# Kernel tuning notes

Hardware: AMD Instinct MI355X
Metric: run time of the kernel (lower is better)

The kernel has to match this reference:

```python
import jax, jax.numpy as jnp
import numpy as np

N_STATIONS = 35
N_PER_ST = 12
N_NODES = N_STATIONS * N_PER_ST   # 420
MAX_EDGES = 5120                  # true edge count = 34 * 12^2 = 4896
MAX_SUPER = 65536                 # true superedge candidates = 33*12*144 = 57024
PI = float(np.pi)

# constraint rows (r, phi, z) from the torch module
C_LO = jnp.array([269.0, -3.15, -2386.0], dtype=jnp.float32)
C_HI = jnp.array([581.0, 3.15, 2386.0], dtype=jnp.float32)


def _calc_dphi(p1, p2):
    d = p2 - p1
    d = jnp.where(d > PI, d - 2.0 * PI, d)
    return jnp.where(d < -PI, d + 2.0 * PI, d)


def _norm_node(v, k):
    return 2.0 * (v - C_LO[k]) / (C_HI[k] - C_LO[k]) - 1.0


def _norm_edge(v, k):
    return 2.0 * v / (C_HI[k] - C_LO[k])


def setup_inputs() -> dict:
    rng = np.random.default_rng(0)
    r = rng.uniform(270.0, 580.0, N_NODES)
    phi = rng.uniform(-3.1, 3.1, N_NODES)
    z = rng.uniform(-2000.0, 2000.0, N_NODES)
    station = np.arange(N_NODES) // N_PER_ST
    track = np.arange(N_NODES) % N_PER_ST  # one hit per track per station
    data = np.stack([
        np.zeros(N_NODES),          # event
        r * np.sin(phi),            # x (so atan2(x, y) = phi)
        r * np.cos(phi),            # y
        z,                          # z
        station.astype(np.float64),
        track.astype(np.float64),
        np.arange(N_NODES, dtype=np.float64),  # index_old
    ], axis=1).astype(np.float32)
    return {"event_data": jnp.asarray(data)}


def reference(event_data):
    x, y, z = event_data[:, 1], event_data[:, 2], event_data[:, 3]
    station, track, index_old = event_data[:, 4], event_data[:, 5], event_data[:, 6]
    # convert() : cartesian -> cylindrical (x<-r, y<-phi)
    r = jnp.sqrt(x * x + y * y)
    phi = jnp.arctan2(x, y)
    # get_graph(): adjacency of consecutive stations, row-major nonzero like torch
    adj = station[:, None] == (station[None, :] - 1.0)
    i_idx, j_idx = jnp.nonzero(adj, size=MAX_EDGES, fill_value=0)
    e_valid = jnp.arange(MAX_EDGES) < jnp.sum(adj)
    phi_p, phi_c = phi[i_idx], phi[j_idx]
    z_p, z_c = z[i_idx], z[j_idx]
    r_p, r_c = r[i_idx], r[j_idx]
    io_p, io_c = index_old[i_idx], index_old[j_idx]
    is_true = track[i_idx] == track[j_idx]  # torch leaves is_true uninitialized; defined as same-track
    dphi = _calc_dphi(phi_p, phi_c)
    dz, dx = z_c - z_p, r_c - r_p
    ez = (station[i_idx] + 1.0) / N_STATIONS
    e_index = jnp.arange(MAX_EDGES, dtype=event_data.dtype)
    # normalize() node-mode on endpoint phi/z (the only normalized cols used later) and edge-mode on dx,dy,dz
    yp_n, yc_n = _norm_node(phi_p, 1), _norm_node(phi_c, 1)
    zp_n, zc_n = _norm_node(z_p, 2), _norm_node(z_c, 2)
    dx_n, dy_n, dz_n = _norm_edge(dx, 0), _norm_edge(dphi, 1), _norm_edge(dz, 2)
    # apply_edge_restriction (masking instead of compaction)
    e_keep = e_valid & (dy_n > -10.0) & (dy_n < 10.0) & (dz_n > -10.0) & (dz_n < 10.0)
    # get_edges_from_supernodes: join first.index_old_c == second.index_old_p
    eq = (io_c[:, None] == io_p[None, :]) & e_keep[:, None] & e_keep[None, :]
    si, sj = jnp.nonzero(eq, size=MAX_SUPER, fill_value=0)
    s_valid = jnp.arange(MAX_SUPER) < jnp.sum(eq)
    d_first = jnp.stack([dx_n[si], dy_n[si], dz_n[si]], -1)
    d_second = jnp.stack([dx_n[sj], dy_n[sj], dz_n[sj]], -1)
    weight = jnp.linalg.norm(d_first - d_second, axis=1)
    # apply_weight_restriction: compact, order-preserving
    s_keep = s_valid & (weight < 0.1)
    (k_idx,) = jnp.nonzero(s_keep, size=MAX_SUPER, fill_value=0)
    k_valid = jnp.arange(MAX_SUPER) < jnp.sum(s_keep)
    fi, se = si[k_idx], sj[k_idx]
    su_is_true = is_true[fi] & is_true[se]
    su_ioc = jnp.where(k_valid, e_index[fi], -2.0)  # superedge index_old_c = first edge's index
    su_iop = jnp.where(k_valid, e_index[se], -2.0)  # superedge index_old_p = second edge's index
    su_y = jnp.where(k_valid, su_is_true.astype(event_data.dtype), 0.0)
    # construct_output_graph: nodes = (filtered) edges, edges = superedges
    node_idx = jnp.where(e_keep, e_index, -1.0)
    X = jnp.where(e_keep[:, None], jnp.stack([yp_n, yc_n, zp_n, zc_n, ez], -1), 0.0)
    Ri = node_idx[:, None] == su_ioc[None, :]   # [MAX_EDGES, MAX_SUPER] bool
    Ro = node_idx[:, None] == su_iop[None, :]
    super_ids = jnp.stack([su_iop, su_ioc], -1)
    edge_ids = jnp.where(e_keep[:, None], jnp.stack([io_p, io_c, e_index], -1), -1.0)
    return X, Ri, Ro, su_y, super_ids, node_idx, edge_ids
```

## Files before the change

kernel.cpp:

```cpp
#include <hip/hip_runtime.h>
#include <math.h>

#define NND 420
#define MAXE 5120
#define MAXS 65536

#define OFF_X    ((size_t)0)
#define OFF_RI   ((size_t)25600)
#define OFF_RO   ((size_t)25600 + 335544320)
#define OFF_SUY  ((size_t)671114240)
#define OFF_SIDS ((size_t)671179776)
#define OFF_NIDX ((size_t)671310848)
#define OFF_EIDS ((size_t)671315968)
#define OUT_TOTAL ((size_t)671331328)

static __device__ __forceinline__ float f32(double d) { return (float)d; }

__device__ float g_dxn[MAXE], g_dyn[MAXE], g_dzn[MAXE];
__device__ float g_iop[MAXE], g_ioc[MAXE];
__device__ int   g_keep[MAXE], g_istrue[MAXE], g_jn[MAXE];
__device__ int   g_estart[NND + 1];
__device__ int   g_cnt2[MAXE], g_off2[MAXE];
__device__ int   g_nedges, g_nkeep;

__global__ __launch_bounds__(512) void kA(const float* __restrict__ ev,
                                          float* __restrict__ out) {
    __shared__ float s_r[NND], s_phi[NND], s_z[NND], s_st[NND], s_trk[NND], s_io[NND];
    __shared__ int   s_cnt[NND];
    __shared__ int   s_off[NND + 1];
    __shared__ short s_ei[MAXE], s_ej[MAXE];

    const float PI_F  = f32(3.141592653589793);
    const float TPI_F = f32(6.283185307179586);
    const float LO1 = -3.15f, SPAN1 = 3.15f + 3.15f;
    const float LO2 = -2386.0f, SPAN2 = 4772.0f;
    const float SPAN0 = 312.0f;

    int t = threadIdx.x;
    for (int n = t; n < NND; n += 512) {
        float x = ev[n * 7 + 1], y = ev[n * 7 + 2];
        s_z[n]   = ev[n * 7 + 3];
        s_st[n]  = ev[n * 7 + 4];
        s_trk[n] = ev[n * 7 + 5];
        s_io[n]  = ev[n * 7 + 6];
        s_r[n]   = sqrtf(__fadd_rn(__fmul_rn(x, x), __fmul_rn(y, y)));
        s_phi[n] = atan2f(x, y);
    }
    __syncthreads();

    for (int i = t; i < NND; i += 512) {
        float target = s_st[i] + 1.0f;
        int c = 0;
        for (int j = 0; j < NND; ++j) c += (s_st[j] == target) ? 1 : 0;
        s_cnt[i] = c;
    }
    __syncthreads();
    if (t == 0) {
        int acc = 0;
        for (int i = 0; i < NND; ++i) { s_off[i] = acc; acc += s_cnt[i]; }
        s_off[NND] = acc;
        g_nedges = acc;
        for (int n = 0; n <= NND; ++n)
            g_estart[n] = (s_off[n] > MAXE) ? MAXE : s_off[n];
    }
    __syncthreads();

    for (int i = t; i < NND; i += 512) {
        float target = s_st[i] + 1.0f;
        int k = s_off[i];
        for (int j = 0; j < NND; ++j) {
            if (s_st[j] == target) {
                if (k < MAXE) { s_ei[k] = (short)i; s_ej[k] = (short)j; }
                ++k;
            }
        }
    }
    __syncthreads();

    int nedges = s_off[NND]; if (nedges > MAXE) nedges = MAXE;

    for (int k = t; k < MAXE; k += 512) {
        bool valid = (k < nedges);
        int i = valid ? (int)s_ei[k] : 0;
        int j = valid ? (int)s_ej[k] : 0;
        float phip = s_phi[i], phic = s_phi[j];
        float zp = s_z[i], zc = s_z[j];
        float rp = s_r[i], rc = s_r[j];
        float iop = s_io[i], ioc = s_io[j];
        int istrue = (s_trk[i] == s_trk[j]) ? 1 : 0;

        float d = __fsub_rn(phic, phip);
        if (d >  PI_F) d = __fsub_rn(d, TPI_F);
        if (d < -PI_F) d = __fadd_rn(d, TPI_F);

        float dzv = __fsub_rn(zc, zp);
        float dxv = __fsub_rn(rc, rp);
        float dxn = __fdiv_rn(__fmul_rn(2.0f, dxv), SPAN0);
        float dyn = __fdiv_rn(__fmul_rn(2.0f, d),   SPAN1);
        float dzn = __fdiv_rn(__fmul_rn(2.0f, dzv), SPAN2);

        bool keep = valid && (dyn > -10.0f) && (dyn < 10.0f)
                          && (dzn > -10.0f) && (dzn < 10.0f);

        float ypn = __fsub_rn(__fdiv_rn(__fmul_rn(2.0f, __fsub_rn(phip, LO1)), SPAN1), 1.0f);
        float ycn = __fsub_rn(__fdiv_rn(__fmul_rn(2.0f, __fsub_rn(phic, LO1)), SPAN1), 1.0f);
        float zpn = __fsub_rn(__fdiv_rn(__fmul_rn(2.0f, __fsub_rn(zp, LO2)), SPAN2), 1.0f);
        float zcn = __fsub_rn(__fdiv_rn(__fmul_rn(2.0f, __fsub_rn(zc, LO2)), SPAN2), 1.0f);
        float ez  = __fdiv_rn(__fadd_rn(s_st[i], 1.0f), 35.0f);

        if (keep) {
            size_t oX = OFF_X + (size_t)k * 5;
            out[oX + 0] = ypn; out[oX + 1] = ycn; out[oX + 2] = zpn;
            out[oX + 3] = zcn; out[oX + 4] = ez;
        }
        out[OFF_NIDX + (size_t)k] = keep ? (float)k : -1.0f;
        size_t oE = OFF_EIDS + (size_t)k * 3;
        out[oE + 0] = keep ? iop : -1.0f;
        out[oE + 1] = keep ? ioc : -1.0f;
        out[oE + 2] = keep ? (float)k : -1.0f;

        g_dxn[k] = dxn; g_dyn[k] = dyn; g_dzn[k] = dzn;
        g_iop[k] = iop; g_ioc[k] = ioc;
        g_keep[k] = keep ? 1 : 0; g_istrue[k] = istrue; g_jn[k] = j;
    }
}

__global__ __launch_bounds__(256) void kB() {
    int a = blockIdx.x * 256 + threadIdx.x;
    if (a >= MAXE) return;
    int c = 0;
    if (g_keep[a]) {
        int jn = g_jn[a];
        float ioca = g_ioc[a];
        float a0 = g_dxn[a], a1 = g_dyn[a], a2 = g_dzn[a];
        int b0 = g_estart[jn], b1 = g_estart[jn + 1];
        for (int b = b0; b < b1; ++b) {
            if (g_keep[b] && (g_iop[b] == ioca)) {
                float d0 = __fsub_rn(a0, g_dxn[b]);
                float d1 = __fsub_rn(a1, g_dyn[b]);
                float d2 = __fsub_rn(a2, g_dzn[b]);
                float w = sqrtf(__fadd_rn(__fadd_rn(__fmul_rn(d0, d0),
                                                    __fmul_rn(d1, d1)),
                                          __fmul_rn(d2, d2)));
                if (w < 0.1f) ++c;
            }
        }
    }
    g_cnt2[a] = c;
}

__global__ __launch_bounds__(1024) void kC() {
    __shared__ int part[1024];
    int t = threadIdx.x;
    int v[5]; int s = 0;
#pragma unroll
    for (int q = 0; q < 5; ++q) { v[q] = g_cnt2[t * 5 + q]; s += v[q]; }
    part[t] = s;
    __syncthreads();
    for (int off = 1; off < 1024; off <<= 1) {
        int x = (t >= off) ? part[t - off] : 0;
        __syncthreads();
        part[t] += x;
        __syncthreads();
    }
    int run = part[t] - s;
#pragma unroll
    for (int q = 0; q < 5; ++q) { g_off2[t * 5 + q] = run; run += v[q]; }
    if (t == 1023) g_nkeep = part[1023];
}

__global__ __launch_bounds__(256) void kD(float* __restrict__ out) {
    int a = blockIdx.x * 256 + threadIdx.x;
    if (a >= MAXE) return;
    if (!g_keep[a]) return;
    int pos = g_off2[a];
    int jn = g_jn[a];
    float ioca = g_ioc[a];
    float a0 = g_dxn[a], a1 = g_dyn[a], a2 = g_dzn[a];
    int b0 = g_estart[jn], b1 = g_estart[jn + 1];
    for (int b = b0; b < b1; ++b) {
        if (g_keep[b] && (g_iop[b] == ioca)) {
            float d0 = __fsub_rn(a0, g_dxn[b]);
            float d1 = __fsub_rn(a1, g_dyn[b]);
            float d2 = __fsub_rn(a2, g_dzn[b]);
            float w = sqrtf(__fadd_rn(__fadd_rn(__fmul_rn(d0, d0),
                                                __fmul_rn(d1, d1)),
                                      __fmul_rn(d2, d2)));
            if (w < 0.1f) {
                if (pos < MAXS) {
                    out[OFF_SUY + (size_t)pos] =
                        (g_istrue[a] && g_istrue[b]) ? 1.0f : 0.0f;
                    size_t os = OFF_SIDS + (size_t)pos * 2;
                    out[os + 0] = (float)b;
                    out[os + 1] = (float)a;
                    out[OFF_RI + (size_t)a * MAXS + (size_t)pos] = 1.0f;
                    out[OFF_RO + (size_t)b * MAXS + (size_t)pos] = 1.0f;
                }
                ++pos;
            }
        }
    }
}

__global__ __launch_bounds__(256) void kE(float* __restrict__ out) {
    int p = blockIdx.x * 256 + threadIdx.x;
    if (p >= MAXS) return;
    if (p >= g_nkeep) {
        size_t os = OFF_SIDS + (size_t)p * 2;
        out[os + 0] = -2.0f;
        out[os + 1] = -2.0f;
    }
}

extern "C" void kernel_launch(void* const* d_in, const int* in_sizes, int n_in,
                              void* d_out, int out_size, void* d_ws, size_t ws_size,
                              hipStream_t stream) {
    const float* ev = (const float*)d_in[0];
    float* out = (float*)d_out;

    hipMemsetAsync(d_out, 0, (size_t)out_size * sizeof(float), stream);

    hipLaunchKernelGGL(kA, dim3(1), dim3(512), 0, stream, ev, out);
    hipLaunchKernelGGL(kB, dim3((MAXE + 255) / 256), dim3(256), 0, stream);
    hipLaunchKernelGGL(kC, dim3(1), dim3(1024), 0, stream);
    hipLaunchKernelGGL(kD, dim3((MAXE + 255) / 256), dim3(256), 0, stream, out);
    hipLaunchKernelGGL(kE, dim3((MAXS + 255) / 256), dim3(256), 0, stream, out);
}
```

Baseline: 2.618 ms.

## Fuse pipeline into one cooperative kernel with in-kernel zero-fill and wave-parallel superedges

Replaces the memset and five kernels with a single cooperative kernel separated by grid syncs. Block 0 builds the edges while the other blocks zero the ~2.7GB output with float4 stores, writing -2 directly into the super_ids region so the separate fill kernel is no longer needed. Superedge counting and emission move from one thread per edge to one wave per edge, using ballot and popcount to compact positions. The output writes are still dominated by the memset-sized store volume, and grid.sync plus using 1023 blocks for the fill may or may not match hipMemset bandwidth.

```diff
diff --git a/kernel.cpp b/kernel.cpp
--- a/kernel.cpp
+++ b/kernel.cpp
@@ -1,5 +1,8 @@
 #include <hip/hip_runtime.h>
+#include <hip/hip_cooperative_groups.h>
 #include <math.h>
+
+namespace cg = cooperative_groups;
 
 #define NND 420
 #define MAXE 5120
@@ -7,28 +10,35 @@
 
 #define OFF_X    ((size_t)0)
 #define OFF_RI   ((size_t)25600)
-#define OFF_RO   ((size_t)25600 + 335544320)
+#define OFF_RO   ((size_t)(25600 + 335544320))
 #define OFF_SUY  ((size_t)671114240)
 #define OFF_SIDS ((size_t)671179776)
 #define OFF_NIDX ((size_t)671310848)
 #define OFF_EIDS ((size_t)671315968)
-#define OUT_TOTAL ((size_t)671331328)
+
+typedef float f4 __attribute__((ext_vector_type(4)));
 
 static __device__ __forceinline__ float f32(double d) { return (float)d; }
 
-__device__ float g_dxn[MAXE], g_dyn[MAXE], g_dzn[MAXE];
-__device__ float g_iop[MAXE], g_ioc[MAXE];
-__device__ int   g_keep[MAXE], g_istrue[MAXE], g_jn[MAXE];
+__device__ float g_phi[NND], g_z[NND], g_st[NND];
+__device__ short g_ei[MAXE], g_ej[MAXE];
 __device__ int   g_estart[NND + 1];
+__device__ float g_dxn[MAXE], g_dyn[MAXE], g_dzn[MAXE], g_iop[MAXE], g_ioc[MAXE];
+__device__ int   g_keep[MAXE], g_istrue[MAXE];
 __device__ int   g_cnt2[MAXE], g_off2[MAXE];
-__device__ int   g_nedges, g_nkeep;
-
-__global__ __launch_bounds__(512) void kA(const float* __restrict__ ev,
-                                          float* __restrict__ out) {
+__device__ int   g_ne;
+
+#define GRID_BLOCKS 1024
+#define NWAVES ((GRID_BLOCKS * 256) >> 6)
+
+__global__ __launch_bounds__(256, 4) void kCoop(const float* __restrict__ ev,
+                                                float* __restrict__ out, int n4) {
+    cg::grid_group grid = cg::this_grid();
+
     __shared__ float s_r[NND], s_phi[NND], s_z[NND], s_st[NND], s_trk[NND], s_io[NND];
-    __shared__ int   s_cnt[NND];
-    __shared__ int   s_off[NND + 1];
+    __shared__ int   s_scan[NND];
     __shared__ short s_ei[MAXE], s_ej[MAXE];
+    __shared__ int   s_part[256];
 
     const float PI_F  = f32(3.141592653589793);
     const float TPI_F = f32(6.283185307179586);
@@ -36,179 +46,201 @@
     const float LO2 = -2386.0f, SPAN2 = 4772.0f;
     const float SPAN0 = 312.0f;
 
-    int t = threadIdx.x;
-    for (int n = t; n < NND; n += 512) {
-        float x = ev[n * 7 + 1], y = ev[n * 7 + 2];
-        s_z[n]   = ev[n * 7 + 3];
-        s_st[n]  = ev[n * 7 + 4];
-        s_trk[n] = ev[n * 7 + 5];
-        s_io[n]  = ev[n * 7 + 6];
-        s_r[n]   = sqrtf(__fadd_rn(__fmul_rn(x, x), __fmul_rn(y, y)));
-        s_phi[n] = atan2f(x, y);
-    }
-    __syncthreads();
-
-    for (int i = t; i < NND; i += 512) {
-        float target = s_st[i] + 1.0f;
+    const int t   = threadIdx.x;
+    const int bid = blockIdx.x;
+
+    if (bid == 0) {
+        for (int n = t; n < NND; n += 256) {
+            float x = ev[n * 7 + 1], y = ev[n * 7 + 2];
+            s_r[n]   = sqrtf(__fadd_rn(__fmul_rn(x, x), __fmul_rn(y, y)));
+            s_phi[n] = atan2f(x, y);
+            s_z[n]   = ev[n * 7 + 3];
+            s_st[n]  = ev[n * 7 + 4];
+            s_trk[n] = ev[n * 7 + 5];
+            s_io[n]  = ev[n * 7 + 6];
+        }
+        __syncthreads();
+        for (int i = t; i < NND; i += 256) {
+            float target = s_st[i] + 1.0f;
+            int c = 0;
+            for (int j = 0; j < NND; ++j) c += (s_st[j] == target) ? 1 : 0;
+            s_scan[i] = c;
+        }
+        __syncthreads();
+        if (t == 0) {
+            int acc = 0;
+            for (int i = 0; i < NND; ++i) {
+                int c = s_scan[i];
+                s_scan[i] = acc;
+                g_estart[i] = acc > MAXE ? MAXE : acc;
+                acc += c;
+            }
+            g_estart[NND] = acc > MAXE ? MAXE : acc;
+            g_ne = acc > MAXE ? MAXE : acc;
+        }
+        __syncthreads();
+        for (int i = t; i < NND; i += 256) {
+            float target = s_st[i] + 1.0f;
+            int k = s_scan[i];
+            for (int j = 0; j < NND; ++j) {
+                if (s_st[j] == target) {
+                    if (k < MAXE) { s_ei[k] = (short)i; s_ej[k] = (short)j; }
+                    ++k;
+                }
+            }
+        }
+        __syncthreads();
+        const int ne = g_ne;
+        for (int k = t; k < MAXE; k += 256) {
+            bool valid = (k < ne);
+            int i = valid ? (int)s_ei[k] : 0;
+            int j = valid ? (int)s_ej[k] : 0;
+            float phip = s_phi[i], phic = s_phi[j];
+            float zp = s_z[i], zc = s_z[j];
+            float rp = s_r[i], rc = s_r[j];
+
+            float d = __fsub_rn(phic, phip);
+            if (d >  PI_F) d = __fsub_rn(d, TPI_F);
+            if (d < -PI_F) d = __fadd_rn(d, TPI_F);
+
+            float dzv = __fsub_rn(zc, zp);
+            float dxv = __fsub_rn(rc, rp);
+            float dxn = __fdiv_rn(__fmul_rn(2.0f, dxv), SPAN0);
+            float dyn = __fdiv_rn(__fmul_rn(2.0f, d),   SPAN1);
+            float dzn = __fdiv_rn(__fmul_rn(2.0f, dzv), SPAN2);
+
+            bool keep = valid && (dyn > -10.0f) && (dyn < 10.0f)
+                              && (dzn > -10.0f) && (dzn < 10.0f);
+
+            g_dxn[k] = dxn; g_dyn[k] = dyn; g_dzn[k] = dzn;
+            g_iop[k] = s_io[i]; g_ioc[k] = s_io[j];
+            g_keep[k] = keep ? 1 : 0;
+            g_istrue[k] = (s_trk[i] == s_trk[j]) ? 1 : 0;
+            g_ei[k] = valid ? s_ei[k] : (short)0;
+            g_ej[k] = valid ? s_ej[k] : (short)0;
+        }
+        for (int n = t; n < NND; n += 256) {
+            g_phi[n] = s_phi[n]; g_z[n] = s_z[n]; g_st[n] = s_st[n];
+        }
+    } else {
+        const size_t LOq = OFF_SIDS >> 2;
+        const size_t HIq = (OFF_SIDS + 2 * (size_t)MAXS) >> 2;
+        f4* p = (f4*)out;
+        const f4 z = {0.f, 0.f, 0.f, 0.f};
+        const f4 m = {-2.f, -2.f, -2.f, -2.f};
+        size_t i = (size_t)(bid - 1) * 256 + t;
+        const size_t stride = (size_t)(GRID_BLOCKS - 1) * 256;
+        for (; i < (size_t)n4; i += stride)
+            p[i] = (i >= LOq && i < HIq) ? m : z;
+    }
+    grid.sync();
+
+    const int gtid = bid * 256 + t;
+    const int wid = gtid >> 6, lane = gtid & 63;
+    const int ne = g_ne;
+    for (int a = wid; a < MAXE; a += NWAVES) {
+        bool akeep = (a < ne) && (g_keep[a] != 0);
         int c = 0;
-        for (int j = 0; j < NND; ++j) c += (s_st[j] == target) ? 1 : 0;
-        s_cnt[i] = c;
-    }
-    __syncthreads();
-    if (t == 0) {
-        int acc = 0;
-        for (int i = 0; i < NND; ++i) { s_off[i] = acc; acc += s_cnt[i]; }
-        s_off[NND] = acc;
-        g_nedges = acc;
-        for (int n = 0; n <= NND; ++n)
-            g_estart[n] = (s_off[n] > MAXE) ? MAXE : s_off[n];
-    }
-    __syncthreads();
-
-    for (int i = t; i < NND; i += 512) {
-        float target = s_st[i] + 1.0f;
-        int k = s_off[i];
-        for (int j = 0; j < NND; ++j) {
-            if (s_st[j] == target) {
-                if (k < MAXE) { s_ei[k] = (short)i; s_ej[k] = (short)j; }
-                ++k;
-            }
-        }
-    }
-    __syncthreads();
-
-    int nedges = s_off[NND]; if (nedges > MAXE) nedges = MAXE;
-
-    for (int k = t; k < MAXE; k += 512) {
-        bool valid = (k < nedges);
-        int i = valid ? (int)s_ei[k] : 0;
-        int j = valid ? (int)s_ej[k] : 0;
-        float phip = s_phi[i], phic = s_phi[j];
-        float zp = s_z[i], zc = s_z[j];
-        float rp = s_r[i], rc = s_r[j];
-        float iop = s_io[i], ioc = s_io[j];
-        int istrue = (s_trk[i] == s_trk[j]) ? 1 : 0;
-
-        float d = __fsub_rn(phic, phip);
-        if (d >  PI_F) d = __fsub_rn(d, TPI_F);
-        if (d < -PI_F) d = __fadd_rn(d, TPI_F);
-
-        float dzv = __fsub_rn(zc, zp);
-        float dxv = __fsub_rn(rc, rp);
-        float dxn = __fdiv_rn(__fmul_rn(2.0f, dxv), SPAN0);
-        float dyn = __fdiv_rn(__fmul_rn(2.0f, d),   SPAN1);
-        float dzn = __fdiv_rn(__fmul_rn(2.0f, dzv), SPAN2);
-
-        bool keep = valid && (dyn > -10.0f) && (dyn < 10.0f)
-                          && (dzn > -10.0f) && (dzn < 10.0f);
-
-        float ypn = __fsub_rn(__fdiv_rn(__fmul_rn(2.0f, __fsub_rn(phip, LO1)), SPAN1), 1.0f);
-        float ycn = __fsub_rn(__fdiv_rn(__fmul_rn(2.0f, __fsub_rn(phic, LO1)), SPAN1), 1.0f);
-        float zpn = __fsub_rn(__fdiv_rn(__fmul_rn(2.0f, __fsub_rn(zp, LO2)), SPAN2), 1.0f);
-        float zcn = __fsub_rn(__fdiv_rn(__fmul_rn(2.0f, __fsub_rn(zc, LO2)), SPAN2), 1.0f);
-        float ez  = __fdiv_rn(__fadd_rn(s_st[i], 1.0f), 35.0f);
-
-        if (keep) {
-            size_t oX = OFF_X + (size_t)k * 5;
-            out[oX + 0] = ypn; out[oX + 1] = ycn; out[oX + 2] = zpn;
-            out[oX + 3] = zcn; out[oX + 4] = ez;
-        }
-        out[OFF_NIDX + (size_t)k] = keep ? (float)k : -1.0f;
-        size_t oE = OFF_EIDS + (size_t)k * 3;
-        out[oE + 0] = keep ? iop : -1.0f;
-        out[oE + 1] = keep ? ioc : -1.0f;
-        out[oE + 2] = keep ? (float)k : -1.0f;
-
-        g_dxn[k] = dxn; g_dyn[k] = dyn; g_dzn[k] = dzn;
-        g_iop[k] = iop; g_ioc[k] = ioc;
-        g_keep[k] = keep ? 1 : 0; g_istrue[k] = istrue; g_jn[k] = j;
-    }
-}
-
-__global__ __launch_bounds__(256) void kB() {
-    int a = blockIdx.x * 256 + threadIdx.x;
-    if (a >= MAXE) return;
-    int c = 0;
-    if (g_keep[a]) {
-        int jn = g_jn[a];
+        float ioca = 0.f, a0 = 0.f, a1 = 0.f, a2 = 0.f;
+        if (akeep) {
+            int jn = (int)g_ej[a];
+            int b0 = g_estart[jn], b1 = g_estart[jn + 1];
+            ioca = g_ioc[a]; a0 = g_dxn[a]; a1 = g_dyn[a]; a2 = g_dzn[a];
+            for (int cs = b0; cs < b1; cs += 64) {
+                int b = cs + lane;
+                bool pred = false;
+                if (b < b1 && g_keep[b] && (g_iop[b] == ioca)) {
+                    float d0 = __fsub_rn(a0, g_dxn[b]);
+                    float d1 = __fsub_rn(a1, g_dyn[b]);
+                    float d2 = __fsub_rn(a2, g_dzn[b]);
+                    float w = sqrtf(__fadd_rn(__fadd_rn(__fmul_rn(d0, d0),
+                                                        __fmul_rn(d1, d1)),
+                                              __fmul_rn(d2, d2)));
+                    pred = (w < 0.1f);
+                }
+                c += (int)__popcll(__ballot(pred));
+            }
+        }
+        if (lane == 0) {
+            g_cnt2[a] = c;
+            if (akeep) {
+                int i = (int)g_ei[a], j = (int)g_ej[a];
+                float phip = g_phi[i], phic = g_phi[j];
+                float zp = g_z[i], zc = g_z[j];
+                float ypn = __fsub_rn(__fdiv_rn(__fmul_rn(2.0f, __fsub_rn(phip, LO1)), SPAN1), 1.0f);
+                float ycn = __fsub_rn(__fdiv_rn(__fmul_rn(2.0f, __fsub_rn(phic, LO1)), SPAN1), 1.0f);
+                float zpn = __fsub_rn(__fdiv_rn(__fmul_rn(2.0f, __fsub_rn(zp, LO2)), SPAN2), 1.0f);
+                float zcn = __fsub_rn(__fdiv_rn(__fmul_rn(2.0f, __fsub_rn(zc, LO2)), SPAN2), 1.0f);
+                float ez  = __fdiv_rn(__fadd_rn(g_st[i], 1.0f), 35.0f);
+                size_t oX = OFF_X + (size_t)a * 5;
+                out[oX + 0] = ypn; out[oX + 1] = ycn; out[oX + 2] = zpn;
+                out[oX + 3] = zcn; out[oX + 4] = ez;
+                out[OFF_NIDX + (size_t)a] = (float)a;
+                size_t oE = OFF_EIDS + (size_t)a * 3;
+                out[oE + 0] = ioca == ioca ? g_iop[a] : g_iop[a];
+                out[oE + 1] = g_ioc[a];
+                out[oE + 2] = (float)a;
+            } else {
+                out[OFF_NIDX + (size_t)a] = -1.0f;
+                size_t oE = OFF_EIDS + (size_t)a * 3;
+                out[oE + 0] = -1.0f; out[oE + 1] = -1.0f; out[oE + 2] = -1.0f;
+            }
+        }
+    }
+    grid.sync();
+
+    if (bid == 0) {
+        int v[20]; int ssum = 0;
+#pragma unroll
+        for (int q = 0; q < 20; ++q) { v[q] = g_cnt2[t * 20 + q]; ssum += v[q]; }
+        s_part[t] = ssum;
+        __syncthreads();
+        for (int off = 1; off < 256; off <<= 1) {
+            int x = (t >= off) ? s_part[t - off] : 0;
+            __syncthreads();
+            s_part[t] += x;
+            __syncthreads();
+        }
+        int run = s_part[t] - ssum;
+#pragma unroll
+        for (int q = 0; q < 20; ++q) { g_off2[t * 20 + q] = run; run += v[q]; }
+    }
+    grid.sync();
+
+    for (int a = wid; a < MAXE; a += NWAVES) {
+        if (!((a < ne) && (g_keep[a] != 0))) continue;
+        int jn = (int)g_ej[a];
+        int b0 = g_estart[jn], b1 = g_estart[jn + 1];
         float ioca = g_ioc[a];
         float a0 = g_dxn[a], a1 = g_dyn[a], a2 = g_dzn[a];
-        int b0 = g_estart[jn], b1 = g_estart[jn + 1];
-        for (int b = b0; b < b1; ++b) {
-            if (g_keep[b] && (g_iop[b] == ioca)) {
+        int ia = g_istrue[a];
+        int base = g_off2[a];
+        for (int cs = b0; cs < b1; cs += 64) {
+            int b = cs + lane;
+            bool pred = false;
+            if (b < b1 && g_keep[b] && (g_iop[b] == ioca)) {
                 float d0 = __fsub_rn(a0, g_dxn[b]);
                 float d1 = __fsub_rn(a1, g_dyn[b]);
                 float d2 = __fsub_rn(a2, g_dzn[b]);
                 float w = sqrtf(__fadd_rn(__fadd_rn(__fmul_rn(d0, d0),
                                                     __fmul_rn(d1, d1)),
                                           __fmul_rn(d2, d2)));
-                if (w < 0.1f) ++c;
-            }
-        }
-    }
-    g_cnt2[a] = c;
-}
-
-__global__ __launch_bounds__(1024) void kC() {
-    __shared__ int part[1024];
-    int t = threadIdx.x;
-    int v[5]; int s = 0;
-#pragma unroll
-    for (int q = 0; q < 5; ++q) { v[q] = g_cnt2[t * 5 + q]; s += v[q]; }
-    part[t] = s;
-    __syncthreads();
-    for (int off = 1; off < 1024; off <<= 1) {
-        int x = (t >= off) ? part[t - off] : 0;
-        __syncthreads();
-        part[t] += x;
-        __syncthreads();
-    }
-    int run = part[t] - s;
-#pragma unroll
-    for (int q = 0; q < 5; ++q) { g_off2[t * 5 + q] = run; run += v[q]; }
-    if (t == 1023) g_nkeep = part[1023];
-}
-
-__global__ __launch_bounds__(256) void kD(float* __restrict__ out) {
-    int a = blockIdx.x * 256 + threadIdx.x;
-    if (a >= MAXE) return;
-    if (!g_keep[a]) return;
-    int pos = g_off2[a];
-    int jn = g_jn[a];
-    float ioca = g_ioc[a];
-    float a0 = g_dxn[a], a1 = g_dyn[a], a2 = g_dzn[a];
-    int b0 = g_estart[jn], b1 = g_estart[jn + 1];
-    for (int b = b0; b < b1; ++b) {
-        if (g_keep[b] && (g_iop[b] == ioca)) {
-            float d0 = __fsub_rn(a0, g_dxn[b]);
-            float d1 = __fsub_rn(a1, g_dyn[b]);
-            float d2 = __fsub_rn(a2, g_dzn[b]);
-            float w = sqrtf(__fadd_rn(__fadd_rn(__fmul_rn(d0, d0),
-                                                __fmul_rn(d1, d1)),
-                                      __fmul_rn(d2, d2)));
-            if (w < 0.1f) {
+                pred = (w < 0.1f);
+            }
+            unsigned long long mask = __ballot(pred);
+            if (pred) {
+                int pos = base + (int)__popcll(mask & ((1ull << lane) - 1ull));
                 if (pos < MAXS) {
-                    out[OFF_SUY + (size_t)pos] =
-                        (g_istrue[a] && g_istrue[b]) ? 1.0f : 0.0f;
+                    out[OFF_SUY + (size_t)pos] = (ia && g_istrue[b]) ? 1.0f : 0.0f;
                     size_t os = OFF_SIDS + (size_t)pos * 2;
                     out[os + 0] = (float)b;
                     out[os + 1] = (float)a;
                     out[OFF_RI + (size_t)a * MAXS + (size_t)pos] = 1.0f;
                     out[OFF_RO + (size_t)b * MAXS + (size_t)pos] = 1.0f;
                 }
-                ++pos;
-            }
-        }
-    }
-}
-
-__global__ __launch_bounds__(256) void kE(float* __restrict__ out) {
-    int p = blockIdx.x * 256 + threadIdx.x;
-    if (p >= MAXS) return;
-    if (p >= g_nkeep) {
-        size_t os = OFF_SIDS + (size_t)p * 2;
-        out[os + 0] = -2.0f;
-        out[os + 1] = -2.0f;
+            }
+            base += (int)__popcll(mask);
+        }
     }
 }
 
@@ -217,12 +249,9 @@
                               hipStream_t stream) {
     const float* ev = (const float*)d_in[0];
     float* out = (float*)d_out;
-
-    hipMemsetAsync(d_out, 0, (size_t)out_size * sizeof(float), stream);
-
-    hipLaunchKernelGGL(kA, dim3(1), dim3(512), 0, stream, ev, out);
-    hipLaunchKernelGGL(kB, dim3((MAXE + 255) / 256), dim3(256), 0, stream);
-    hipLaunchKernelGGL(kC, dim3(1), dim3(1024), 0, stream);
-    hipLaunchKernelGGL(kD, dim3((MAXE + 255) / 256), dim3(256), 0, stream, out);
-    hipLaunchKernelGGL(kE, dim3((MAXS + 255) / 256), dim3(256), 0, stream, out);
+    int n4 = out_size / 4;
+
+    void* args[] = { (void*)&ev, (void*)&out, (void*)&n4 };
+    hipLaunchCooperativeKernel((const void*)kCoop, dim3(GRID_BLOCKS), dim3(256),
+                               args, 0, stream);
 }
```

New measurement: 2.923 ms. +11.6%, slower.
